# Optimization experiments

Hardware: AMD Instinct MI355X
Metric: run time of the kernel (lower is better)

## Reference

```python
import jax, jax.numpy as jnp
import numpy as np

SR = 2            # search_range
LEAK = 0.2        # keras.activations.leaky_relu default negative_slope


def _conv(x, k, b):
    y = jax.lax.conv_general_dilated(x, k, (1, 1), 'SAME',
                                     dimension_numbers=('NHWC', 'HWIO', 'NHWC'))
    return y + b


def _lrelu(x):
    return jnp.where(x >= 0, x, LEAK * x)


def _bilinear_sample(imgs, cx, cy):
    # Faithful to the keras BilinearSampler: indices are PIXEL-flat (b*H*W + y*W + x)
    # but keras.ops.take flattens imgs over ALL dims (incl. channels), so the gather
    # reads from imgs.reshape(-1) at those pixel-flat positions and output has 1 channel.
    B, H, W, C = imgs.shape
    x0 = jnp.floor(cx); x1 = x0 + 1.0
    y0 = jnp.floor(cy); y1 = y0 + 1.0
    wt_x0 = x1 - cx; wt_x1 = cx - x0
    wt_y0 = y1 - cy; wt_y1 = cy - y0
    x_max = float(W - 1); y_max = float(H - 1)
    x0s = jnp.clip(x0, 0.0, x_max); x1s = jnp.clip(x1, 0.0, x_max)
    y0s = jnp.clip(y0, 0.0, y_max); y1s = jnp.clip(y1, 0.0, y_max)
    dim2 = float(W)
    base = (jnp.arange(B, dtype=jnp.float32) * float(H * W)).reshape(B, 1, 1, 1)
    by0 = base + y0s * dim2
    by1 = base + y1s * dim2
    flat = imgs.reshape(-1)
    g = lambda idx: jnp.take(flat, idx.astype(jnp.int32))
    im00 = g(x0s + by0); im01 = g(x0s + by1)
    im10 = g(x1s + by0); im11 = g(x1s + by1)
    return (wt_x0 * wt_y0) * im00 + (wt_x0 * wt_y1) * im01 \
         + (wt_x1 * wt_y0) * im10 + (wt_x1 * wt_y1) * im11


def _module_m(left, right, prev_disp, params):
    B, H, W, C = left.shape
    # upsample previous disparity to this level's resolution (bilinear, half-pixel)
    up = jax.image.resize(prev_disp, (B, H, W, 1), method='bilinear')
    # build sampling coords: x = j - flow, y = i (flow y-component is zeros)
    jj = jnp.arange(W, dtype=jnp.float32).reshape(1, 1, W, 1)
    ii = jnp.arange(H, dtype=jnp.float32).reshape(1, H, 1, 1)
    cx = jj - up                                   # [B,H,W,1]
    cy = jnp.broadcast_to(ii, (B, H, W, 1))        # [B,H,W,1]
    warped = _bilinear_sample(right, cx, cy)       # [B,H,W,1]
    # cost volume: shifted products, channel-mean (warped broadcasts over C)
    padded = jnp.pad(warped, ((0, 0), (0, 0), (SR, SR), (0, 0)))
    costs = [jnp.mean(left * padded[:, :, i:W + i, :], axis=3, keepdims=True)
             for i in range(2 * SR + 1)]
    cost_curve = jnp.concatenate([left] + costs, axis=-1)   # [B,H,W,C+5]
    vol = jnp.concatenate([cost_curve, up], axis=-1)        # [B,H,W,C+6]
    x = _lrelu(_conv(vol, params['k1'], params['b1']))
    x = _lrelu(_conv(x, params['k2'], params['b2']))
    x = _lrelu(_conv(x, params['k3'], params['b3']))
    x = _lrelu(_conv(x, params['k4'], params['b4']))
    x = _lrelu(_conv(x, params['k5'], params['b5']))
    x = _conv(x, params['k6'], params['b6'])                # linear head -> [B,H,W,1]
    return x


def setup_inputs() -> dict:
    key = jax.random.key(0)
    ks = jax.random.split(key, 16)
    B, H, W, C = 8, 128, 256, 128
    left = jax.random.normal(ks[0], (B, H, W, C), dtype=jnp.float32)
    right = jax.random.normal(ks[1], (B, H, W, C), dtype=jnp.float32)
    prev_disp = jax.random.uniform(ks[2], (B, H // 2, W // 2, 1), dtype=jnp.float32) * 8.0
    in_ch = C + (2 * SR + 1) + 1  # 134
    chans = [(in_ch, 128), (128, 128), (128, 96), (96, 64), (64, 32), (32, 1)]
    inp = {'left': left, 'right': right, 'prev_disp': prev_disp}
    for i, (ci, co) in enumerate(chans, start=1):
        inp[f'k{i}'] = jax.random.normal(ks[2 + 2 * i], (3, 3, ci, co), dtype=jnp.float32) * 0.05
        inp[f'b{i}'] = jnp.zeros((co,), dtype=jnp.float32)
    return inp


def reference(left, right, prev_disp, k1, b1, k2, b2, k3, b3, k4, b4, k5, b5, k6, b6):
    params = {'k1': k1, 'b1': b1, 'k2': k2, 'b2': b2, 'k3': k3, 'b3': b3,
              'k4': k4, 'b4': b4, 'k5': k5, 'b5': b5, 'k6': k6, 'b6': b6}
    return _module_m(left, right, prev_disp, params)
```

## Files before the change

### kernel.cpp

```cpp
#include <hip/hip_runtime.h>

typedef __attribute__((ext_vector_type(8))) short short8;
typedef __attribute__((ext_vector_type(4))) float f32x4;
typedef __attribute__((ext_vector_type(4))) unsigned short us4;

#define LEAK 0.2f

__device__ __forceinline__ float b2f(unsigned short s) {
    unsigned u = ((unsigned)s) << 16;
    return __builtin_bit_cast(float, u);
}
__device__ __forceinline__ unsigned short f2b(float f) {
    unsigned u = __builtin_bit_cast(unsigned, f);
    u += 0x7fffu + ((u >> 16) & 1u);
    return (unsigned short)(u >> 16);
}

__device__ __forceinline__ void async16(const short* g, short* l) {
    __builtin_amdgcn_global_load_lds(
        (const __attribute__((address_space(1))) void*)g,
        (__attribute__((address_space(3))) void*)l, 16, 0, 0);
}


__device__ __forceinline__ float up_at(const float* __restrict__ pd, int b, int i, int j) {
    float sy = i * 0.5f - 0.25f;
    float sx = j * 0.5f - 0.25f;
    float fy0 = floorf(sy), fx0 = floorf(sx);
    float fy = sy - fy0, fx = sx - fx0;
    int y0 = (int)fy0, x0 = (int)fx0;
    int y0c = min(max(y0, 0), 63), y1c = min(max(y0 + 1, 0), 63);
    int x0c = min(max(x0, 0), 127), x1c = min(max(x0 + 1, 0), 127);
    const float* p = pd + b * 64 * 128;
    float v00 = p[y0c * 128 + x0c], v01 = p[y0c * 128 + x1c];
    float v10 = p[y1c * 128 + x0c], v11 = p[y1c * 128 + x1c];
    return (1.f - fy) * ((1.f - fx) * v00 + fx * v01) + fy * ((1.f - fx) * v10 + fx * v11);
}

__device__ __forceinline__ float warp_at(const float* __restrict__ right,
                                         const float* __restrict__ pd, int b, int i, int j) {
    float up = up_at(pd, b, i, j);
    float cx = (float)j - up;
    float x0 = floorf(cx), x1 = x0 + 1.f;
    float w0 = x1 - cx, w1 = cx - x0;
    float x0s = fminf(fmaxf(x0, 0.f), 255.f);
    float x1s = fminf(fmaxf(x1, 0.f), 255.f);
    float base = (float)(b * 32768 + i * 256);
    int i0 = (int)(x0s + base);
    int i1 = (int)(x1s + base);
    return w0 * right[i0] + w1 * right[i1];
}

__global__ void prep_kernel(const float* __restrict__ left, const float* __restrict__ right,
                            const float* __restrict__ pd, short* __restrict__ vol) {
    int idx = blockIdx.x * 256 + threadIdx.x;
    int w = idx & 255, h = (idx >> 8) & 127, b = idx >> 15;
    const float* lp = left + (size_t)idx * 128;
    short* vp = vol + ((size_t)(b * 130 + h + 1) * 258 + (w + 1)) * 144;
    float sum = 0.f;
#pragma unroll 8
    for (int c = 0; c < 128; c += 4) {
        float4 v = *(const float4*)(lp + c);
        sum += (v.x + v.y) + (v.z + v.w);
        us4 o;
        o.x = f2b(v.x); o.y = f2b(v.y); o.z = f2b(v.z); o.w = f2b(v.w);
        *(us4*)(vp + c) = o;
    }
    float meanleft = sum * (1.f / 128.f);
    float up = up_at(pd, b, h, w);
#pragma unroll
    for (int t = 0; t < 5; ++t) {
        int jj = w + t - 2;
        float cost = 0.f;
        if (jj >= 0 && jj < 256) cost = warp_at(right, pd, b, h, jj) * meanleft;
        vp[128 + t] = (short)f2b(cost);
    }
    vp[133] = (short)f2b(up);
#pragma unroll
    for (int c = 134; c < 144; c += 2) { vp[c] = 0; vp[c + 1] = 0; }
}

__global__ void halo_zero_one(short* __restrict__ buf, int C) {
    int nchunk = C >> 3;
    int slot = blockIdx.x * 256 + threadIdx.x;
    int total = 8 * 772 * nchunk;
    if (slot >= total) return;
    int chunk = slot % nchunk;
    int pix = slot / nchunk;
    int b = pix / 772, p = pix % 772;
    int row, col;
    if (p < 516) { row = (p < 258) ? 0 : 129; col = (p < 258) ? p : p - 258; }
    else { int q = p - 516; row = 1 + (q >> 1); col = (q & 1) ? 257 : 0; }
    short8 z = {};
    *(short8*)(buf + ((size_t)(b * 130 + row) * 258 + col) * C + chunk * 8) = z;
}

__global__ void wconv_kernel(const float* __restrict__ k, short* __restrict__ wt,
                             int CIN, int COUT, int KC) {
    int idx = blockIdx.x * 256 + threadIdx.x;
    int total = 9 * KC * COUT * 32;
    if (idx >= total) return;
    int kk = idx & 31;
    int rest = idx >> 5;
    int n = rest % COUT; rest /= COUT;
    int tap = rest % 9, kc = rest / 9;
    int ci = kc * 32 + kk;
    float v = (ci < CIN) ? k[(size_t)(tap * CIN + ci) * COUT + n] : 0.f;
    wt[idx] = (short)f2b(v);
}

template <int KC, int CIN_STR, int COUT, int NT, int LASTC>
__launch_bounds__(512, 2)
__global__ void conv3x3_kernel(const short* __restrict__ in, const short* __restrict__ wt,
                               const float* __restrict__ bias, short* __restrict__ out) {
    __shared__ short ldsA[6 * 130 * 4 * 8];
    __shared__ short ldsW[9 * COUT * 32];
    const int WSLOTS = 9 * COUT * 4;
    const int WSTRIDE = 9 * COUT * 32;

    int t = threadIdx.x;
    int lane = t & 63, wid = t >> 6;
    int q = lane >> 4, col = lane & 15;
    int out_row = wid >> 1, col_off = (wid & 1) << 6;

    int wtile = blockIdx.x & 1;
    int rest = blockIdx.x >> 1;
    int htile = rest & 31, b = rest >> 5;
    int w0h = wtile << 7;
    int row0 = htile << 2;

    const short* inbase = in + ((size_t)(b * 130 + row0) * 258 + w0h) * CIN_STR;

    f32x4 acc[4][NT] = {};

    for (int kc = 0; kc < KC; ++kc) {
        for (int i = t; i < 3120; i += 512) {
            int r = i / 520, rem = i % 520;
            int p = rem >> 2, s = rem & 3;
            int c = (s - p) & 3;
            if (LASTC == 4 || kc < KC - 1 || c < LASTC) {
                const short* g = inbase + ((size_t)r * 258 + p) * CIN_STR + kc * 32 + c * 8;
                async16(g, ldsA + (size_t)(i & ~63) * 8);
            }
        }
        {
            const short* wsrc = wt + (size_t)kc * WSTRIDE;
            for (int i = t; i < WSLOTS; i += 512)
                async16(wsrc + (size_t)i * 8, ldsW + (size_t)(i & ~63) * 8);
        }
        __syncthreads();

#pragma unroll
        for (int dy = 0; dy < 3; ++dy) {
#pragma unroll
            for (int dx = 0; dx < 3; ++dx) {
                int ldsrow = out_row + dy;
                short8 a[4], bfr[NT];
#pragma unroll
                for (int mt = 0; mt < 4; ++mt) {
                    int p = col_off + mt * 16 + col + dx;
                    a[mt] = *(const short8*)(ldsA +
                        (size_t)(((ldsrow * 130 + p) << 2) + ((q + p) & 3)) * 8);
                }
                const short* wp = ldsW + (size_t)(dy * 3 + dx) * COUT * 32;
#pragma unroll
                for (int nt = 0; nt < NT; ++nt)
                    bfr[nt] = *(const short8*)(wp + (nt * 16 + col) * 32 + q * 8);
#pragma unroll
                for (int mt = 0; mt < 4; ++mt)
#pragma unroll
                    for (int nt = 0; nt < NT; ++nt)
                        acc[mt][nt] = __builtin_amdgcn_mfma_f32_16x16x32_bf16(
                            a[mt], bfr[nt], acc[mt][nt], 0, 0, 0);
            }
        }
        __syncthreads();
    }

    size_t obase = ((size_t)(b * 130 + row0 + 1 + out_row) * 258 + (w0h + 1 + col_off)) * COUT;
#pragma unroll
    for (int nt = 0; nt < NT; ++nt) {
        int n = nt * 16 + col;
        float bv = bias[n];
#pragma unroll
        for (int mt = 0; mt < 4; ++mt) {
#pragma unroll
            for (int rr = 0; rr < 4; ++rr) {
                int m = mt * 16 + q * 4 + rr;
                float v = acc[mt][nt][rr] + bv;
                v = (v >= 0.f) ? v : LEAK * v;
                out[obase + (size_t)m * COUT + n] = (short)f2b(v);
            }
        }
    }
}

__global__ void conv6_kernel(const short* __restrict__ x, const float* __restrict__ k,
                             const float* __restrict__ bias, float* __restrict__ out) {
    __shared__ float wk[288];
    int t = threadIdx.x;
    for (int i = t; i < 288; i += 256) wk[i] = k[i];
    __syncthreads();
    int idx = blockIdx.x * 256 + t;
    int w = idx & 255, h = (idx >> 8) & 127, b = idx >> 15;
    float acc = bias[0];
#pragma unroll
    for (int dy = 0; dy < 3; ++dy) {
#pragma unroll
        for (int dx = 0; dx < 3; ++dx) {
            const short* xp = x + ((size_t)(b * 130 + h + dy) * 258 + (w + dx)) * 32;
            const float* wp = wk + (dy * 3 + dx) * 32;
#pragma unroll
            for (int c8 = 0; c8 < 4; ++c8) {
                short8 v = *(const short8*)(xp + c8 * 8);
#pragma unroll
                for (int j = 0; j < 8; ++j)
                    acc += b2f((unsigned short)v[j]) * wp[c8 * 8 + j];
            }
        }
    }
    out[idx] = acc;
}

extern "C" void kernel_launch(void* const* d_in, const int* in_sizes, int n_in,
                              void* d_out, int out_size, void* d_ws, size_t ws_size,
                              hipStream_t stream) {
    const float* left  = (const float*)d_in[0];
    const float* right = (const float*)d_in[1];
    const float* pd    = (const float*)d_in[2];
    const float* k[6];
    const float* bb[6];
    for (int i = 0; i < 6; ++i) { k[i] = (const float*)d_in[3 + 2 * i]; bb[i] = (const float*)d_in[4 + 2 * i]; }

    char* ws = (char*)d_ws;
    short* wt1 = (short*)ws;
    short* wt2 = (short*)(ws + 368640);
    short* wt3 = (short*)(ws + 663552);
    short* wt4 = (short*)(ws + 884736);
    short* wt5 = (short*)(ws + 995328);
    short* vol = (short*)(ws + 1048576);
    short* X1  = (short*)(ws + 1048576 + 77276160);
    short* X2  = vol;
    short* X3  = X1;
    short* X4  = vol;
    short* X5  = X1;

    auto hz = [&](short* buf, int C) {
        int blocks = (8 * 772 * (C >> 3) + 255) / 256;
        halo_zero_one<<<blocks, 256, 0, stream>>>(buf, C);
    };

    prep_kernel<<<1024, 256, 0, stream>>>(left, right, pd, vol);
    wconv_kernel<<<720, 256, 0, stream>>>(k[0], wt1, 134, 128, 5);
    wconv_kernel<<<576, 256, 0, stream>>>(k[1], wt2, 128, 128, 4);
    wconv_kernel<<<432, 256, 0, stream>>>(k[2], wt3, 128, 96, 4);
    wconv_kernel<<<216, 256, 0, stream>>>(k[3], wt4, 96, 64, 3);
    wconv_kernel<<<72,  256, 0, stream>>>(k[4], wt5, 64, 32, 2);
    hz(vol, 144);
    hz(X1, 128);

    conv3x3_kernel<5, 144, 128, 8, 2><<<512, 512, 0, stream>>>(vol, wt1, bb[0], X1);
    hz(X2, 128);
    conv3x3_kernel<4, 128, 128, 8, 4><<<512, 512, 0, stream>>>(X1, wt2, bb[1], X2);
    hz(X3, 96);
    conv3x3_kernel<4, 128,  96, 6, 4><<<512, 512, 0, stream>>>(X2, wt3, bb[2], X3);
    hz(X4, 64);
    conv3x3_kernel<3,  96,  64, 4, 4><<<512, 512, 0, stream>>>(X3, wt4, bb[3], X4);
    hz(X5, 32);
    conv3x3_kernel<2,  64,  32, 2, 4><<<512, 512, 0, stream>>>(X4, wt5, bb[4], X5);
    conv6_kernel<<<1024, 256, 0, stream>>>(X5, k[5], bb[5], (float*)d_out);
}
```

Baseline: 697.1 us.

## Stage prep inputs through LDS for coalesced loads and stores; batch weight conversions

The prep kernel now gives each block a 64-pixel row segment. It loads left features, the right image row and two prev_disp rows into shared memory with coalesced float4 loads. Four threads share each pixel and combine the channel mean with shuffles, and the bf16 output tile is written to global memory with wide contiguous stores instead of strided per-thread accesses. The five weight-conversion launches are merged into a single 2D-grid launch to cut launch overhead. This uses about 54KB of LDS per block, which may limit occupancy, and the merged launch idles many blocks for the smaller layers.

Result: faster. 628.2 us (-9.9%).

```diff
diff --git a/kernel.cpp b/kernel.cpp
--- a/kernel.cpp
+++ b/kernel.cpp
@@ -22,62 +22,98 @@
         (__attribute__((address_space(3))) void*)l, 16, 0, 0);
 }
 
-
-__device__ __forceinline__ float up_at(const float* __restrict__ pd, int b, int i, int j) {
-    float sy = i * 0.5f - 0.25f;
-    float sx = j * 0.5f - 0.25f;
-    float fy0 = floorf(sy), fx0 = floorf(sx);
-    float fy = sy - fy0, fx = sx - fx0;
-    int y0 = (int)fy0, x0 = (int)fx0;
+__global__ __launch_bounds__(256)
+void prep_kernel(const float* __restrict__ left, const float* __restrict__ right,
+                 const float* __restrict__ pd, short* __restrict__ vol) {
+    __shared__ __align__(16) float inL[64 * 132];
+    __shared__ __align__(16) float rrow[256];
+    __shared__ __align__(16) float pr0[128];
+    __shared__ __align__(16) float pr1[128];
+    __shared__ __align__(16) short outT[64 * 144];
+
+    int t = threadIdx.x;
+    int blk = blockIdx.x;
+    int wq = blk & 3, h = (blk >> 2) & 127, b = blk >> 9;
+    int w0 = wq << 6;
+
+    float sy = h * 0.5f - 0.25f;
+    float fy0 = floorf(sy);
+    float fy = sy - fy0;
+    int y0 = (int)fy0;
     int y0c = min(max(y0, 0), 63), y1c = min(max(y0 + 1, 0), 63);
-    int x0c = min(max(x0, 0), 127), x1c = min(max(x0 + 1, 0), 127);
-    const float* p = pd + b * 64 * 128;
-    float v00 = p[y0c * 128 + x0c], v01 = p[y0c * 128 + x1c];
-    float v10 = p[y1c * 128 + x0c], v11 = p[y1c * 128 + x1c];
-    return (1.f - fy) * ((1.f - fx) * v00 + fx * v01) + fy * ((1.f - fx) * v10 + fx * v11);
-}
-
-__device__ __forceinline__ float warp_at(const float* __restrict__ right,
-                                         const float* __restrict__ pd, int b, int i, int j) {
-    float up = up_at(pd, b, i, j);
-    float cx = (float)j - up;
-    float x0 = floorf(cx), x1 = x0 + 1.f;
-    float w0 = x1 - cx, w1 = cx - x0;
-    float x0s = fminf(fmaxf(x0, 0.f), 255.f);
-    float x1s = fminf(fmaxf(x1, 0.f), 255.f);
-    float base = (float)(b * 32768 + i * 256);
-    int i0 = (int)(x0s + base);
-    int i1 = (int)(x1s + base);
-    return w0 * right[i0] + w1 * right[i1];
-}
-
-__global__ void prep_kernel(const float* __restrict__ left, const float* __restrict__ right,
-                            const float* __restrict__ pd, short* __restrict__ vol) {
-    int idx = blockIdx.x * 256 + threadIdx.x;
-    int w = idx & 255, h = (idx >> 8) & 127, b = idx >> 15;
-    const float* lp = left + (size_t)idx * 128;
-    short* vp = vol + ((size_t)(b * 130 + h + 1) * 258 + (w + 1)) * 144;
+
+    const float* lp = left + ((size_t)((b * 128 + h) * 256 + w0)) * 128;
+#pragma unroll
+    for (int k2 = 0; k2 < 8; ++k2) {
+        int g = t + k2 * 256;
+        int p = g >> 5, j = g & 31;
+        float4 v = *(const float4*)(lp + (size_t)g * 4);
+        *(float4*)(&inL[p * 132 + j * 4]) = v;
+    }
+    if (t < 64) {
+        *(float4*)(&rrow[t * 4]) =
+            *(const float4*)(right + ((size_t)(b * 128 + h)) * 256 + t * 4);
+    } else if (t < 96) {
+        int i2 = t - 64;
+        *(float4*)(&pr0[i2 * 4]) = *(const float4*)(pd + (size_t)(b * 64 + y0c) * 128 + i2 * 4);
+    } else if (t < 128) {
+        int i2 = t - 96;
+        *(float4*)(&pr1[i2 * 4]) = *(const float4*)(pd + (size_t)(b * 64 + y1c) * 128 + i2 * 4);
+    }
+    __syncthreads();
+
+    int p = t >> 2, s = t & 3;
+    int w = w0 + p;
+    const float* src = &inL[p * 132 + s * 32];
+    short* odst = &outT[p * 144 + s * 32];
     float sum = 0.f;
-#pragma unroll 8
-    for (int c = 0; c < 128; c += 4) {
-        float4 v = *(const float4*)(lp + c);
-        sum += (v.x + v.y) + (v.z + v.w);
+#pragma unroll
+    for (int i = 0; i < 8; ++i) {
+        float f0 = src[i * 4], f1 = src[i * 4 + 1], f2 = src[i * 4 + 2], f3 = src[i * 4 + 3];
+        sum += (f0 + f1) + (f2 + f3);
         us4 o;
-        o.x = f2b(v.x); o.y = f2b(v.y); o.z = f2b(v.z); o.w = f2b(v.w);
-        *(us4*)(vp + c) = o;
-    }
-    float meanleft = sum * (1.f / 128.f);
-    float up = up_at(pd, b, h, w);
-#pragma unroll
-    for (int t = 0; t < 5; ++t) {
-        int jj = w + t - 2;
-        float cost = 0.f;
-        if (jj >= 0 && jj < 256) cost = warp_at(right, pd, b, h, jj) * meanleft;
-        vp[128 + t] = (short)f2b(cost);
-    }
-    vp[133] = (short)f2b(up);
-#pragma unroll
-    for (int c = 134; c < 144; c += 2) { vp[c] = 0; vp[c + 1] = 0; }
+        o.x = f2b(f0); o.y = f2b(f1); o.z = f2b(f2); o.w = f2b(f3);
+        *(us4*)(odst + i * 4) = o;
+    }
+    sum += __shfl_xor(sum, 1);
+    sum += __shfl_xor(sum, 2);
+    float mean = sum * (1.f / 128.f);
+
+    float one_fy = 1.f - fy;
+#pragma unroll
+    for (int tap = s; tap < 5; tap += 4) {
+        int jj = w + tap - 2;
+        if (jj >= 0 && jj < 256) {
+            float sx = jj * 0.5f - 0.25f;
+            float fx0 = floorf(sx);
+            float fx = sx - fx0;
+            int x0 = (int)fx0;
+            int x0c = min(max(x0, 0), 127), x1c = min(max(x0 + 1, 0), 127);
+            float up = one_fy * ((1.f - fx) * pr0[x0c] + fx * pr0[x1c])
+                     + fy     * ((1.f - fx) * pr1[x0c] + fx * pr1[x1c]);
+            float cx = (float)jj - up;
+            float xf0 = floorf(cx), xf1 = xf0 + 1.f;
+            float w0x = xf1 - cx, w1x = cx - xf0;
+            int ix0 = (int)fminf(fmaxf(xf0, 0.f), 255.f);
+            int ix1 = (int)fminf(fmaxf(xf1, 0.f), 255.f);
+            float warped = w0x * rrow[ix0] + w1x * rrow[ix1];
+            outT[p * 144 + 128 + tap] = (short)f2b(warped * mean);
+            if (tap == 2) outT[p * 144 + 133] = (short)f2b(up);
+        } else {
+            outT[p * 144 + 128 + tap] = 0;
+        }
+    }
+    if (s == 0) { outT[p * 144 + 134] = 0; outT[p * 144 + 135] = 0; }
+    if (s == 3) {
+        us4 z = {};
+        *(us4*)(&outT[p * 144 + 136]) = z;
+        *(us4*)(&outT[p * 144 + 140]) = z;
+    }
+    __syncthreads();
+
+    short* gdst = vol + ((size_t)(b * 130 + h + 1) * 258 + (w0 + 1)) * 144;
+    for (int g = t; g < 1152; g += 256)
+        *(short8*)(gdst + g * 8) = *(const short8*)(&outT[g * 8]);
 }
 
 __global__ void halo_zero_one(short* __restrict__ buf, int C) {
@@ -95,8 +131,21 @@
     *(short8*)(buf + ((size_t)(b * 130 + row) * 258 + col) * C + chunk * 8) = z;
 }
 
-__global__ void wconv_kernel(const float* __restrict__ k, short* __restrict__ wt,
-                             int CIN, int COUT, int KC) {
+__global__ void wconv_all(const float* __restrict__ k1, const float* __restrict__ k2,
+                          const float* __restrict__ k3, const float* __restrict__ k4,
+                          const float* __restrict__ k5,
+                          short* __restrict__ w1, short* __restrict__ w2,
+                          short* __restrict__ w3, short* __restrict__ w4,
+                          short* __restrict__ w5) {
+    const int CINt[5]  = {134, 128, 128, 96, 64};
+    const int COUTt[5] = {128, 128, 96, 64, 32};
+    const int KCt[5]   = {5, 4, 4, 3, 2};
+    const float* srcs[5] = {k1, k2, k3, k4, k5};
+    short* dsts[5] = {w1, w2, w3, w4, w5};
+    int l = blockIdx.y;
+    int CIN = CINt[l], COUT = COUTt[l], KC = KCt[l];
+    const float* k = srcs[l];
+    short* wt = dsts[l];
     int idx = blockIdx.x * 256 + threadIdx.x;
     int total = 9 * KC * COUT * 32;
     if (idx >= total) return;
@@ -250,12 +299,9 @@
         halo_zero_one<<<blocks, 256, 0, stream>>>(buf, C);
     };
 
-    prep_kernel<<<1024, 256, 0, stream>>>(left, right, pd, vol);
-    wconv_kernel<<<720, 256, 0, stream>>>(k[0], wt1, 134, 128, 5);
-    wconv_kernel<<<576, 256, 0, stream>>>(k[1], wt2, 128, 128, 4);
-    wconv_kernel<<<432, 256, 0, stream>>>(k[2], wt3, 128, 96, 4);
-    wconv_kernel<<<216, 256, 0, stream>>>(k[3], wt4, 96, 64, 3);
-    wconv_kernel<<<72,  256, 0, stream>>>(k[4], wt5, 64, 32, 2);
+    prep_kernel<<<4096, 256, 0, stream>>>(left, right, pd, vol);
+    wconv_all<<<dim3(720, 5), 256, 0, stream>>>(k[0], k[1], k[2], k[3], k[4],
+                                                wt1, wt2, wt3, wt4, wt5);
     hz(vol, 144);
     hz(X1, 128);
 
```
